# Optimization experiments

Measured on AMD Instinct MI355X. Metric: run time of the kernel, lower is better.

The kernel has to match this reference:

```python
import jax, jax.numpy as jnp
import numpy as np

N = 4096   # patients
D = 256    # encoding dim per modality
EPS = 1e-8 # torch CosineSimilarity eps


def setup_inputs() -> dict:
    key = jax.random.key(0)
    ks = jax.random.split(key, 7)
    return {
        "log_hazard": jax.random.normal(ks[0], (N,), dtype=jnp.float32),
        "time": jax.random.randint(ks[1], (N,), 0, 3650, dtype=jnp.int32),
        "event": jax.random.randint(ks[2], (N,), 0, 2, dtype=jnp.int32),
        "eb0": jax.random.normal(ks[3], (N, D), dtype=jnp.float32),
        "eb1": jax.random.normal(ks[4], (N, D), dtype=jnp.float32),
        "eb2": jax.random.normal(ks[5], (N, D), dtype=jnp.float32),
        "eb3": jax.random.normal(ks[6], (N, D), dtype=jnp.float32),
        "M_margin": 1,
    }


def _cox_npll(h, t, e):
    # risk_matrix = (outer(t,t) >= t^2).T  ->  risk[i,j] = (t_j * t_i >= t_i^2)
    tt = t[:, None] * t[None, :]                      # [N,N] = t_i * t_j
    risk = (tt >= (t * t)[:, None]).astype(h.dtype)   # row i: patients j with t_j >= t_i
    log_denom = jnp.log(risk @ jnp.exp(h))            # [N]
    ef = e.astype(h.dtype)
    return -jnp.sum(ef * (h - log_denom)) / jnp.sum(ef)


def _similarity_loss(blocks, margin):
    # Vectorized form of the O(N^2 * n_mod) pairwise loop.
    matched = jnp.zeros((N, N), dtype=blocks[0].dtype)  # sum_mod cos(x_i, x_j) over valid mods
    own = jnp.zeros((N, N), dtype=blocks[0].dtype)      # sum_mod cos(x_i, x_i) over valid mods
    for x in blocks:
        nrm = jnp.linalg.norm(x, axis=1)                # [N]
        den = jnp.maximum(nrm, EPS)
        xn = x / den[:, None]
        S = xn @ xn.T                                   # cos(x_i, x_j) with torch eps semantics
        diag = (nrm * nrm) / (den * den)                # cos(x_i, x_i)
        miss = jnp.all(x == x[:, :1], axis=1)           # modality missing (constant row)
        valid = (~(miss[:, None] | miss[None, :])).astype(x.dtype)
        matched = matched + valid * S
        own = own + valid * diag[:, None]
    offdiag = 1.0 - jnp.eye(N, dtype=matched.dtype)
    per_pair = jax.nn.relu(margin - matched + own)
    return jnp.sum(offdiag * per_pair)


def reference(log_hazard, time, event, eb0, eb1, eb2, eb3, M_margin):
    margin = jnp.float32(M_margin)
    cox = _cox_npll(log_hazard, time, event)
    sim = _similarity_loss([eb0, eb1, eb2, eb3], margin)
    return cox + sim
```

## Files before the change

### kernel.cpp

```cpp
#include <hip/hip_runtime.h>
#include <stdint.h>

#define NPAT 4096
#define DIM  256
#define KB   1024
#define EPSV 1e-8f
#define BT   128
#define BKB  256
#define NT   (NPAT / BT)
#define NBLK (NT * (NT + 1) / 2)
#define NBINS 4096

typedef float f32x4 __attribute__((ext_vector_type(4)));

#define WS_DVAL_OFF 256
#define WS_MVEC_OFF (WS_DVAL_OFF + 16*NPAT)
#define WS_XN_OFF   (WS_MVEC_OFF + 16*NPAT)

__device__ __forceinline__ void gl_lds16(const uint8_t* g, uint8_t* l) {
  __builtin_amdgcn_global_load_lds(
      (const __attribute__((address_space(1))) void*)g,
      (__attribute__((address_space(3))) void*)l, 16, 0, 0);
}

__device__ __forceinline__ float decode_margin(const int* pm) {
  int v = *pm;
  if (v > -16777216 && v < 16777216) return (float)v;
  return __int_as_float(v);
}

__global__ __launch_bounds__(256) void prep_kernel(
    const float4* __restrict__ eb0, const float4* __restrict__ eb1,
    const float4* __restrict__ eb2, const float4* __restrict__ eb3,
    uint8_t* __restrict__ Xn, float* __restrict__ dval_f,
    float* __restrict__ mvec_f, float* __restrict__ scal)
{
  const int i    = blockIdx.x;
  const int wv   = threadIdx.x >> 6;
  const int lane = threadIdx.x & 63;
  const float4* ebs[4] = {eb0, eb1, eb2, eb3};
  const float4 v = ebs[wv][i * (DIM / 4) + lane];
  float s = v.x * v.x + v.y * v.y + v.z * v.z + v.w * v.w;
#pragma unroll
  for (int o = 32; o; o >>= 1) s += __shfl_down(s, o, 64);
  s = __shfl(s, 0, 64);
  const float x0 = __shfl(v.x, 0, 64);
  const bool eq = (v.x == x0) && (v.y == x0) && (v.z == x0) && (v.w == x0);
  const bool miss = (__ballot(eq) == ~0ull);
  const float nrm = sqrtf(s);
  const float den = fmaxf(nrm, EPSV);
  const float inv = miss ? 0.0f : (1.0f / den);
  int p = 0;
  p = __builtin_amdgcn_cvt_pk_fp8_f32(v.x * inv, v.y * inv, p, false);
  p = __builtin_amdgcn_cvt_pk_fp8_f32(v.z * inv, v.w * inv, p, true);
  *(int*)&Xn[(size_t)i * KB + wv * DIM + lane * 4] = p;
  if (lane == 0) {
    const float diag = (nrm * nrm) / (den * den);
    dval_f[i * 4 + wv] = miss ? 0.0f : diag;
    mvec_f[i * 4 + wv] = miss ? 0.0f : 1.0f;
  }
  if (i == 0 && threadIdx.x == 0) {
    scal[0] = 0.0f;
    scal[1] = 0.0f;
    ((unsigned*)scal)[2] = 0u;
  }
}

__global__ __launch_bounds__(512, 4) void sim_gemm_kernel(
    const uint8_t* __restrict__ Xn, const float4* __restrict__ dval,
    const float4* __restrict__ mvec, const int* __restrict__ pmargin,
    const float* __restrict__ h, const int* __restrict__ t,
    const int* __restrict__ e, float* __restrict__ scal,
    float* __restrict__ out)
{
  __shared__ __align__(16) uint8_t smem[2 * BT * BKB];
  __shared__ float wred[8];
  uint8_t* lA = smem;
  uint8_t* lB = smem + BT * BKB;

  const int L   = blockIdx.x;
  const int tid = threadIdx.x;
  const int lane = tid & 63, wvv = tid >> 6;

  if (L == NBLK) {
    float* bins = (float*)smem;
    float* wt   = (float*)(smem + 16384);
    float* rn   = (float*)(smem + 16384 + 64);
    float* rd   = (float*)(smem + 16384 + 128);
#pragma unroll
    for (int k = 0; k < 8; ++k) bins[tid + k * 512] = 0.0f;
    __syncthreads();
#pragma unroll
    for (int k = 0; k < 8; ++k) {
      const int i = tid + k * 512;
      atomicAdd(&bins[t[i]], expf(h[i]));
    }
    __syncthreads();
    float seg[8]; float part = 0.0f;
#pragma unroll
    for (int k = 0; k < 8; ++k) { seg[k] = bins[tid * 8 + k]; part += seg[k]; }
    float sfx = part;
#pragma unroll
    for (int off = 1; off < 64; off <<= 1) {
      const float u = __shfl_down(sfx, off, 64);
      if (lane + off < 64) sfx += u;
    }
    if (lane == 0) wt[wvv] = sfx;
    __syncthreads();
    float above = 0.0f;
    for (int w = wvv + 1; w < 8; ++w) above += wt[w];
    float run = above + (sfx - part);
#pragma unroll
    for (int k = 7; k >= 0; --k) { run += seg[k]; bins[tid * 8 + k] = run; }
    __syncthreads();
    float nloc = 0.0f, dloc = 0.0f;
#pragma unroll
    for (int k = 0; k < 8; ++k) {
      const int i = tid + k * 512;
      const float ei = (float)e[i];
      if (ei != 0.0f) { nloc += ei * (h[i] - logf(bins[t[i]])); dloc += ei; }
    }
#pragma unroll
    for (int o = 32; o; o >>= 1) {
      nloc += __shfl_down(nloc, o, 64);
      dloc += __shfl_down(dloc, o, 64);
    }
    if (lane == 0) { rn[wvv] = nloc; rd[wvv] = dloc; }
    __syncthreads();
    if (tid == 0) {
      float n = 0.0f, d = 0.0f;
#pragma unroll
      for (int k = 0; k < 8; ++k) { n += rn[k]; d += rd[k]; }
      atomicExch(&scal[1], n / d);
      __threadfence();
      const unsigned old = atomicAdd(&((unsigned*)scal)[2], 1u);
      if (old == NBLK) {
        __threadfence();
        out[0] = atomicAdd(&scal[0], 0.0f) - (n / d);
      }
    }
    return;
  }

  int bi = (int)((2 * NT + 1 - sqrtf((float)((2 * NT + 1) * (2 * NT + 1)) - 8.0f * L)) * 0.5f);
  if (bi < 0) bi = 0;
  if (bi > NT - 1) bi = NT - 1;
  while (bi > 0 && bi * NT - bi * (bi - 1) / 2 > L) --bi;
  while ((bi + 1) * NT - (bi + 1) * bi / 2 <= L) ++bi;
  const int bj = bi + (L - (bi * NT - bi * (bi - 1) / 2));

  const int wi = wvv >> 1, wj = wvv & 1;
  const int mrow = lane & 15, kg = lane >> 4;
  const int kgh = kg >> 1, half8 = (kg & 1) * 8;

  const int srow   = tid >> 4;
  const int sgoff  = ((tid & 15) ^ (srow & 15)) * 16;
  const uint8_t* gA = Xn + (size_t)(bi * BT) * KB;
  const uint8_t* gB = Xn + (size_t)(bj * BT) * KB;

  f32x4 acc[2][4] = {};
  const int rA0 = wi * 32 + mrow;
  const int rB0 = wj * 64 + mrow;

  for (int kit = 0; kit < 4; ++kit) {
    const int k0 = kit * BKB;
    __syncthreads();
#pragma unroll
    for (int q = 0; q < 4; ++q) {
      const size_t go = (size_t)(q * 32 + srow) * KB + k0 + sgoff;
      gl_lds16(gA + go, &lA[q * 8192 + tid * 16]);
      gl_lds16(gB + go, &lB[q * 8192 + tid * 16]);
    }
    __syncthreads();
#pragma unroll
    for (int s = 0; s < 8; ++s) {
      const int o = (((2 * s + kgh) ^ mrow) << 4) + half8;
      const long a0 = *(const long*)&lA[(rA0)      * BKB + o];
      const long a1 = *(const long*)&lA[(rA0 + 16) * BKB + o];
      long bf[4];
#pragma unroll
      for (int mj = 0; mj < 4; ++mj) bf[mj] = *(const long*)&lB[(rB0 + mj * 16) * BKB + o];
#pragma unroll
      for (int mj = 0; mj < 4; ++mj) {
        acc[0][mj] = __builtin_amdgcn_mfma_f32_16x16x32_fp8_fp8(a0, bf[mj], acc[0][mj], 0, 0, 0);
        acc[1][mj] = __builtin_amdgcn_mfma_f32_16x16x32_fp8_fp8(a1, bf[mj], acc[1][mj], 0, 0, 0);
      }
    }
  }

  __syncthreads();
  float4* eRDi = (float4*)smem;
  float4* eCMi = (float4*)smem + BT;
  float4* eRDj = (float4*)smem + 2 * BT;
  float4* eCMj = (float4*)smem + 3 * BT;
  if (tid < BT) {
    eRDi[tid] = dval[bi * BT + tid];
    eCMi[tid] = mvec[bi * BT + tid];
  } else if (tid < 2 * BT) {
    const int s = tid - BT;
    eRDj[s] = dval[bj * BT + s];
    eCMj[s] = mvec[bj * BT + s];
  }
  __syncthreads();

  const float margin = decode_margin(pmargin);
  const bool isDiag = (bi == bj);
  float local = 0.0f;
  const int rq = (lane >> 4) * 4;
  const int cc = lane & 15;
#pragma unroll
  for (int mi = 0; mi < 2; ++mi) {
#pragma unroll
    for (int mj = 0; mj < 4; ++mj) {
      const int jl = wj * 64 + mj * 16 + cc;
      const float4 cmj = eCMj[jl];
      const float4 rdj = eRDj[jl];
#pragma unroll
      for (int r = 0; r < 4; ++r) {
        const int il = wi * 32 + mi * 16 + rq + r;
        const float4 rdi = eRDi[il];
        const float sv = acc[mi][mj][r];
        const float own_ij = rdi.x * cmj.x + rdi.y * cmj.y + rdi.z * cmj.z + rdi.w * cmj.w;
        const float v1 = fmaxf(margin - sv + own_ij, 0.0f);
        local += (isDiag && il == jl) ? 0.0f : v1;
        if (!isDiag) {
          const float4 cmi = eCMi[il];
          const float own_ji = rdj.x * cmi.x + rdj.y * cmi.y + rdj.z * cmi.z + rdj.w * cmi.w;
          local += fmaxf(margin - sv + own_ji, 0.0f);
        }
      }
    }
  }
#pragma unroll
  for (int o = 32; o; o >>= 1) local += __shfl_down(local, o, 64);
  if (lane == 0) wred[wvv] = local;
  __syncthreads();
  if (tid == 0) {
    float bsum = 0.0f;
#pragma unroll
    for (int k = 0; k < 8; ++k) bsum += wred[k];
    atomicAdd(&scal[0], bsum);
    __threadfence();
    const unsigned old = atomicAdd(&((unsigned*)scal)[2], 1u);
    if (old == NBLK) {
      __threadfence();
      out[0] = atomicAdd(&scal[0], 0.0f) - atomicAdd(&scal[1], 0.0f);
    }
  }
}

extern "C" void kernel_launch(void* const* d_in, const int* in_sizes, int n_in,
                              void* d_out, int out_size, void* d_ws, size_t ws_size,
                              hipStream_t stream) {
  const float* h    = (const float*)d_in[0];
  const int*   t    = (const int*)  d_in[1];
  const int*   e    = (const int*)  d_in[2];
  const float4* eb0 = (const float4*)d_in[3];
  const float4* eb1 = (const float4*)d_in[4];
  const float4* eb2 = (const float4*)d_in[5];
  const float4* eb3 = (const float4*)d_in[6];
  const int*   pm   = (const int*)  d_in[7];

  char*    ws   = (char*)d_ws;
  float*   scal = (float*)ws;
  float*   dvf  = (float*)(ws + WS_DVAL_OFF);
  float*   mvf  = (float*)(ws + WS_MVEC_OFF);
  uint8_t* Xn   = (uint8_t*)(ws + WS_XN_OFF);

  prep_kernel<<<NPAT, 256, 0, stream>>>(eb0, eb1, eb2, eb3, Xn, dvf, mvf, scal);
  sim_gemm_kernel<<<NBLK + 1, 512, 0, stream>>>(Xn, (const float4*)dvf, (const float4*)mvf,
                                                pm, h, t, e, scal, (float*)d_out);
}
```

Baseline: 121.1 us.

## Pre-swizzle FP8 operands into MFMA fragment layout and load directly to registers

The prep kernel now writes the normalized FP8 embeddings in a fragment-major layout matching the 32x32x64 scaled MFMA operand format, so the GEMM kernel loads A/B fragments straight from global memory into registers with double buffering instead of staging through LDS. The block shrinks to 256 threads, each wave computing a 64x64 subtile with 32x32x64 f8f6f4 MFMAs, and the Cox block moves to block 0 so it starts early. This removes LDS traffic and barriers from the main loop. In exchange, A/B reuse across waves now relies on cache instead of shared memory, raising global/L2 traffic and register pressure.

```diff
diff --git a/kernel.cpp b/kernel.cpp
--- a/kernel.cpp
+++ b/kernel.cpp
@@ -3,25 +3,20 @@
 
 #define NPAT 4096
 #define DIM  256
-#define KB   1024
 #define EPSV 1e-8f
 #define BT   128
-#define BKB  256
 #define NT   (NPAT / BT)
 #define NBLK (NT * (NT + 1) / 2)
+#define NSTEP 16
 #define NBINS 4096
 
-typedef float f32x4 __attribute__((ext_vector_type(4)));
+typedef float f32x4  __attribute__((ext_vector_type(4)));
+typedef float f32x16 __attribute__((ext_vector_type(16)));
+typedef int   i32x8  __attribute__((ext_vector_type(8)));
 
 #define WS_DVAL_OFF 256
 #define WS_MVEC_OFF (WS_DVAL_OFF + 16*NPAT)
 #define WS_XN_OFF   (WS_MVEC_OFF + 16*NPAT)
-
-__device__ __forceinline__ void gl_lds16(const uint8_t* g, uint8_t* l) {
-  __builtin_amdgcn_global_load_lds(
-      (const __attribute__((address_space(1))) void*)g,
-      (__attribute__((address_space(3))) void*)l, 16, 0, 0);
-}
 
 __device__ __forceinline__ float decode_margin(const int* pm) {
   int v = *pm;
@@ -32,7 +27,7 @@
 __global__ __launch_bounds__(256) void prep_kernel(
     const float4* __restrict__ eb0, const float4* __restrict__ eb1,
     const float4* __restrict__ eb2, const float4* __restrict__ eb3,
-    uint8_t* __restrict__ Xn, float* __restrict__ dval_f,
+    uint8_t* __restrict__ XnF, float* __restrict__ dval_f,
     float* __restrict__ mvec_f, float* __restrict__ scal)
 {
   const int i    = blockIdx.x;
@@ -53,7 +48,11 @@
   int p = 0;
   p = __builtin_amdgcn_cvt_pk_fp8_f32(v.x * inv, v.y * inv, p, false);
   p = __builtin_amdgcn_cvt_pk_fp8_f32(v.z * inv, v.w * inv, p, true);
-  *(int*)&Xn[(size_t)i * KB + wv * DIM + lane * 4] = p;
+  const int g  = i >> 5, r = i & 31;
+  const int ss = wv * 4 + (lane >> 4);
+  const int h  = (lane >> 3) & 1;
+  const int b  = (lane & 7) * 4;
+  *(int*)&XnF[(size_t)((g * 16 + ss) * 64 + (h * 32 + r)) * 32 + b] = p;
   if (lane == 0) {
     const float diag = (nrm * nrm) / (den * den);
     dval_f[i * 4 + wv] = miss ? 0.0f : diag;
@@ -66,39 +65,35 @@
   }
 }
 
-__global__ __launch_bounds__(512, 4) void sim_gemm_kernel(
-    const uint8_t* __restrict__ Xn, const float4* __restrict__ dval,
+__global__ __launch_bounds__(256, 3) void sim_gemm_kernel(
+    const uint8_t* __restrict__ XnF, const float4* __restrict__ dval,
     const float4* __restrict__ mvec, const int* __restrict__ pmargin,
     const float* __restrict__ h, const int* __restrict__ t,
     const int* __restrict__ e, float* __restrict__ scal,
     float* __restrict__ out)
 {
-  __shared__ __align__(16) uint8_t smem[2 * BT * BKB];
-  __shared__ float wred[8];
-  uint8_t* lA = smem;
-  uint8_t* lB = smem + BT * BKB;
-
+  __shared__ __align__(16) uint8_t smem[16384 + 256];
   const int L   = blockIdx.x;
   const int tid = threadIdx.x;
   const int lane = tid & 63, wvv = tid >> 6;
 
-  if (L == NBLK) {
+  if (L == 0) {
     float* bins = (float*)smem;
     float* wt   = (float*)(smem + 16384);
-    float* rn   = (float*)(smem + 16384 + 64);
-    float* rd   = (float*)(smem + 16384 + 128);
-#pragma unroll
-    for (int k = 0; k < 8; ++k) bins[tid + k * 512] = 0.0f;
-    __syncthreads();
-#pragma unroll
-    for (int k = 0; k < 8; ++k) {
-      const int i = tid + k * 512;
+    float* rn   = (float*)(smem + 16384 + 32);
+    float* rd   = (float*)(smem + 16384 + 64);
+#pragma unroll
+    for (int k = 0; k < 16; ++k) bins[tid + k * 256] = 0.0f;
+    __syncthreads();
+#pragma unroll
+    for (int k = 0; k < 16; ++k) {
+      const int i = tid + k * 256;
       atomicAdd(&bins[t[i]], expf(h[i]));
     }
     __syncthreads();
-    float seg[8]; float part = 0.0f;
-#pragma unroll
-    for (int k = 0; k < 8; ++k) { seg[k] = bins[tid * 8 + k]; part += seg[k]; }
+    float seg[16]; float part = 0.0f;
+#pragma unroll
+    for (int k = 0; k < 16; ++k) { seg[k] = bins[tid * 16 + k]; part += seg[k]; }
     float sfx = part;
 #pragma unroll
     for (int off = 1; off < 64; off <<= 1) {
@@ -108,15 +103,15 @@
     if (lane == 0) wt[wvv] = sfx;
     __syncthreads();
     float above = 0.0f;
-    for (int w = wvv + 1; w < 8; ++w) above += wt[w];
+    for (int w = wvv + 1; w < 4; ++w) above += wt[w];
     float run = above + (sfx - part);
 #pragma unroll
-    for (int k = 7; k >= 0; --k) { run += seg[k]; bins[tid * 8 + k] = run; }
+    for (int k = 15; k >= 0; --k) { run += seg[k]; bins[tid * 16 + k] = run; }
     __syncthreads();
     float nloc = 0.0f, dloc = 0.0f;
 #pragma unroll
-    for (int k = 0; k < 8; ++k) {
-      const int i = tid + k * 512;
+    for (int k = 0; k < 16; ++k) {
+      const int i = tid + k * 256;
       const float ei = (float)e[i];
       if (ei != 0.0f) { nloc += ei * (h[i] - logf(bins[t[i]])); dloc += ei; }
     }
@@ -130,7 +125,7 @@
     if (tid == 0) {
       float n = 0.0f, d = 0.0f;
 #pragma unroll
-      for (int k = 0; k < 8; ++k) { n += rn[k]; d += rd[k]; }
+      for (int k = 0; k < 4; ++k) { n += rn[k]; d += rd[k]; }
       atomicExch(&scal[1], n / d);
       __threadfence();
       const unsigned old = atomicAdd(&((unsigned*)scal)[2], 1u);
@@ -142,84 +137,79 @@
     return;
   }
 
-  int bi = (int)((2 * NT + 1 - sqrtf((float)((2 * NT + 1) * (2 * NT + 1)) - 8.0f * L)) * 0.5f);
+  const int T = L - 1;
+  int bi = (int)((2 * NT + 1 - sqrtf((float)((2 * NT + 1) * (2 * NT + 1)) - 8.0f * T)) * 0.5f);
   if (bi < 0) bi = 0;
   if (bi > NT - 1) bi = NT - 1;
-  while (bi > 0 && bi * NT - bi * (bi - 1) / 2 > L) --bi;
-  while ((bi + 1) * NT - (bi + 1) * bi / 2 <= L) ++bi;
-  const int bj = bi + (L - (bi * NT - bi * (bi - 1) / 2));
+  while (bi > 0 && bi * NT - bi * (bi - 1) / 2 > T) --bi;
+  while ((bi + 1) * NT - (bi + 1) * bi / 2 <= T) ++bi;
+  const int bj = bi + (T - (bi * NT - bi * (bi - 1) / 2));
 
   const int wi = wvv >> 1, wj = wvv & 1;
-  const int mrow = lane & 15, kg = lane >> 4;
-  const int kgh = kg >> 1, half8 = (kg & 1) * 8;
-
-  const int srow   = tid >> 4;
-  const int sgoff  = ((tid & 15) ^ (srow & 15)) * 16;
-  const uint8_t* gA = Xn + (size_t)(bi * BT) * KB;
-  const uint8_t* gB = Xn + (size_t)(bj * BT) * KB;
-
-  f32x4 acc[2][4] = {};
-  const int rA0 = wi * 32 + mrow;
-  const int rB0 = wj * 64 + mrow;
-
-  for (int kit = 0; kit < 4; ++kit) {
-    const int k0 = kit * BKB;
-    __syncthreads();
-#pragma unroll
-    for (int q = 0; q < 4; ++q) {
-      const size_t go = (size_t)(q * 32 + srow) * KB + k0 + sgoff;
-      gl_lds16(gA + go, &lA[q * 8192 + tid * 16]);
-      gl_lds16(gB + go, &lB[q * 8192 + tid * 16]);
-    }
-    __syncthreads();
-#pragma unroll
-    for (int s = 0; s < 8; ++s) {
-      const int o = (((2 * s + kgh) ^ mrow) << 4) + half8;
-      const long a0 = *(const long*)&lA[(rA0)      * BKB + o];
-      const long a1 = *(const long*)&lA[(rA0 + 16) * BKB + o];
-      long bf[4];
-#pragma unroll
-      for (int mj = 0; mj < 4; ++mj) bf[mj] = *(const long*)&lB[(rB0 + mj * 16) * BKB + o];
-#pragma unroll
-      for (int mj = 0; mj < 4; ++mj) {
-        acc[0][mj] = __builtin_amdgcn_mfma_f32_16x16x32_fp8_fp8(a0, bf[mj], acc[0][mj], 0, 0, 0);
-        acc[1][mj] = __builtin_amdgcn_mfma_f32_16x16x32_fp8_fp8(a1, bf[mj], acc[1][mj], 0, 0, 0);
-      }
-    }
-  }
-
-  __syncthreads();
+  const int gA0 = bi * 4 + wi * 2;
+  const int gB0 = bj * 4 + wj * 2;
+  const uint8_t* pA = XnF + (size_t)(gA0 * 16) * 2048 + lane * 32;
+  const uint8_t* pB = XnF + (size_t)(gB0 * 16) * 2048 + lane * 32;
+
+  f32x16 acc[2][2] = {};
+  i32x8 af[2][2], bf[2][2];
+
+#define LOADSTEP(buf, s)                                              \
+  do {                                                                \
+    af[buf][0] = *(const i32x8*)(pA + (size_t)(s) * 2048);            \
+    af[buf][1] = *(const i32x8*)(pA + 32768 + (size_t)(s) * 2048);    \
+    bf[buf][0] = *(const i32x8*)(pB + (size_t)(s) * 2048);            \
+    bf[buf][1] = *(const i32x8*)(pB + 32768 + (size_t)(s) * 2048);    \
+  } while (0)
+
+  LOADSTEP(0, 0);
+#pragma unroll
+  for (int s = 0; s < NSTEP; ++s) {
+    const int c = s & 1;
+    if (s < NSTEP - 1) LOADSTEP(c ^ 1, s + 1);
+#pragma unroll
+    for (int mi = 0; mi < 2; ++mi)
+#pragma unroll
+      for (int mj = 0; mj < 2; ++mj)
+        acc[mi][mj] = __builtin_amdgcn_mfma_scale_f32_32x32x64_f8f6f4(
+            af[c][mi], bf[c][mj], acc[mi][mj],
+            0, 0,
+            0, 0x7F7F7F7F,
+            0, 0x7F7F7F7F);
+  }
+#undef LOADSTEP
+
   float4* eRDi = (float4*)smem;
   float4* eCMi = (float4*)smem + BT;
   float4* eRDj = (float4*)smem + 2 * BT;
   float4* eCMj = (float4*)smem + 3 * BT;
+  float*  wred = (float*)(smem + 8192);
   if (tid < BT) {
     eRDi[tid] = dval[bi * BT + tid];
     eCMi[tid] = mvec[bi * BT + tid];
-  } else if (tid < 2 * BT) {
-    const int s = tid - BT;
-    eRDj[s] = dval[bj * BT + s];
-    eCMj[s] = mvec[bj * BT + s];
+  } else {
+    const int ss = tid - BT;
+    eRDj[ss] = dval[bj * BT + ss];
+    eCMj[ss] = mvec[bj * BT + ss];
   }
   __syncthreads();
 
   const float margin = decode_margin(pmargin);
   const bool isDiag = (bi == bj);
   float local = 0.0f;
-  const int rq = (lane >> 4) * 4;
-  const int cc = lane & 15;
+  const int colA = lane & 31, hsel = lane >> 5;
 #pragma unroll
   for (int mi = 0; mi < 2; ++mi) {
 #pragma unroll
-    for (int mj = 0; mj < 4; ++mj) {
-      const int jl = wj * 64 + mj * 16 + cc;
+    for (int mj = 0; mj < 2; ++mj) {
+      const int jl = wj * 64 + mj * 32 + colA;
       const float4 cmj = eCMj[jl];
       const float4 rdj = eRDj[jl];
 #pragma unroll
-      for (int r = 0; r < 4; ++r) {
-        const int il = wi * 32 + mi * 16 + rq + r;
+      for (int rr = 0; rr < 16; ++rr) {
+        const int il = wi * 64 + mi * 32 + (rr & 3) + 8 * (rr >> 2) + 4 * hsel;
         const float4 rdi = eRDi[il];
-        const float sv = acc[mi][mj][r];
+        const float sv = acc[mi][mj][rr];
         const float own_ij = rdi.x * cmj.x + rdi.y * cmj.y + rdi.z * cmj.z + rdi.w * cmj.w;
         const float v1 = fmaxf(margin - sv + own_ij, 0.0f);
         local += (isDiag && il == jl) ? 0.0f : v1;
@@ -236,10 +226,7 @@
   if (lane == 0) wred[wvv] = local;
   __syncthreads();
   if (tid == 0) {
-    float bsum = 0.0f;
-#pragma unroll
-    for (int k = 0; k < 8; ++k) bsum += wred[k];
-    atomicAdd(&scal[0], bsum);
+    atomicAdd(&scal[0], wred[0] + wred[1] + wred[2] + wred[3]);
     __threadfence();
     const unsigned old = atomicAdd(&((unsigned*)scal)[2], 1u);
     if (old == NBLK) {
@@ -265,9 +252,9 @@
   float*   scal = (float*)ws;
   float*   dvf  = (float*)(ws + WS_DVAL_OFF);
   float*   mvf  = (float*)(ws + WS_MVEC_OFF);
-  uint8_t* Xn   = (uint8_t*)(ws + WS_XN_OFF);
-
-  prep_kernel<<<NPAT, 256, 0, stream>>>(eb0, eb1, eb2, eb3, Xn, dvf, mvf, scal);
-  sim_gemm_kernel<<<NBLK + 1, 512, 0, stream>>>(Xn, (const float4*)dvf, (const float4*)mvf,
+  uint8_t* XnF  = (uint8_t*)(ws + WS_XN_OFF);
+
+  prep_kernel<<<NPAT, 256, 0, stream>>>(eb0, eb1, eb2, eb3, XnF, dvf, mvf, scal);
+  sim_gemm_kernel<<<NBLK + 1, 256, 0, stream>>>(XnF, (const float4*)dvf, (const float4*)mvf,
                                                 pm, h, t, e, scal, (float*)d_out);
 }
```

New measurement: 248.7 us. +105.4%, slower.
